# Performance work log

Hardware: AMD Instinct MI355X
Metric: run time of the kernel (lower is better)

Reference implementation:

```python
import jax, jax.numpy as jnp
import numpy as np
import math

B, H, S, D = 2, 16, 2048, 64

def setup_inputs() -> dict:
    key = jax.random.key(0)
    kq, kk, kv = jax.random.split(key, 3)
    Q = jax.random.normal(kq, (B, H, S, D), dtype=jnp.float32)
    K = jax.random.normal(kk, (B, H, S, D), dtype=jnp.float32)
    V = jax.random.normal(kv, (B, H, S, D), dtype=jnp.float32)
    causal_mask = jnp.tril(jnp.ones((S, S), dtype=bool))
    return {"Q": Q, "K": K, "V": V, "causal_mask": causal_mask}

def reference(Q, K, V, causal_mask):
    d_k = K.shape[-1]
    scores = jnp.einsum('bhqd,bhkd->bhqk', Q, K) / math.sqrt(d_k)
    scores = jnp.where(causal_mask, scores, -jnp.inf)
    probs = jax.nn.softmax(scores, axis=-1)
    return jnp.einsum('bhqk,bhkd->bhqd', probs, V)
```

## Files before the change

### kernel.cpp

```cpp
#include <hip/hip_runtime.h>
#include <math.h>


constexpr int kS   = 2048;
constexpr int kD   = 64;
constexpr int kBH  = 32;
constexpr int kPadP = 72;

typedef short short8 __attribute__((ext_vector_type(8)));
typedef float float4v __attribute__((ext_vector_type(4)));
typedef float float16v __attribute__((ext_vector_type(16)));
typedef unsigned int u32;
typedef unsigned short u16;

static __device__ inline u16 f2bf(float f) {
  union { float f; unsigned u; } v; v.f = f;
  unsigned r = v.u + 0x7FFF + ((v.u >> 16) & 1);
  return (u16)(r >> 16);
}

static __device__ inline short8 pack8(float4v a, float4v b) {
  short8 r;
  r[0] = (short)f2bf(a[0]); r[1] = (short)f2bf(a[1]);
  r[2] = (short)f2bf(a[2]); r[3] = (short)f2bf(a[3]);
  r[4] = (short)f2bf(b[0]); r[5] = (short)f2bf(b[1]);
  r[6] = (short)f2bf(b[2]); r[7] = (short)f2bf(b[3]);
  return r;
}

static __device__ inline void async_cp16(const void* g, void* l) {
  __builtin_amdgcn_global_load_lds(
      (const __attribute__((address_space(1))) u32*)g,
      (__attribute__((address_space(3))) u32*)l, 16, 0, 0);
}

static __device__ inline void swap32(u32 a, u32 b, u32& oa, u32& ob) {
#if __has_builtin(__builtin_amdgcn_permlane32_swap)
  auto r = __builtin_amdgcn_permlane32_swap(a, b, false, false);
  oa = r[0]; ob = r[1];
#else
  asm volatile("v_permlane32_swap_b32 %0, %1" : "+v"(a), "+v"(b));
  oa = a; ob = b;
#endif
}

__global__ __launch_bounds__(256)
void prep_kernel(const float* __restrict__ Q, const float* __restrict__ K,
                 const float* __restrict__ V,
                 u16* __restrict__ Qb, u16* __restrict__ Kb, u16* __restrict__ VT) {
  __shared__ u16 tile[64 * kPadP];
  const int tid = threadIdx.x;
  const int bh = blockIdx.y, st = blockIdx.x;
  const size_t ibase = (size_t)bh * kS * kD + (size_t)st * 64 * kD;
  const int r  = tid >> 2;
  const int c0 = (tid & 3) * 16;
  {
    const float scl = 0.125f * 1.44269504089f;
    const float* qp = Q + ibase + (size_t)r * kD + c0;
    float4v a = *(const float4v*)(qp);
    float4v b = *(const float4v*)(qp + 4);
    float4v c = *(const float4v*)(qp + 8);
    float4v d = *(const float4v*)(qp + 12);
    #pragma unroll
    for (int i = 0; i < 4; ++i) { a[i] *= scl; b[i] *= scl; c[i] *= scl; d[i] *= scl; }
    u16* dst = Qb + ibase + (size_t)r * kD + c0;
    *(short8*)dst       = pack8(a, b);
    *(short8*)(dst + 8) = pack8(c, d);
  }
  {
    const float* kp = K + ibase + (size_t)r * kD + c0;
    float4v a = *(const float4v*)(kp);
    float4v b = *(const float4v*)(kp + 4);
    float4v c = *(const float4v*)(kp + 8);
    float4v d = *(const float4v*)(kp + 12);
    u16* dst = Kb + ibase + (size_t)r * kD + c0;
    *(short8*)dst       = pack8(a, b);
    *(short8*)(dst + 8) = pack8(c, d);
  }
  {
    const float* vp = V + ibase + (size_t)r * kD + c0;
    float4v a = *(const float4v*)(vp);
    float4v b = *(const float4v*)(vp + 4);
    float4v c = *(const float4v*)(vp + 8);
    float4v d = *(const float4v*)(vp + 12);
    u16* t = &tile[r * kPadP + c0];
    *(short8*)t       = pack8(a, b);
    *(short8*)(t + 8) = pack8(c, d);
  }
  __syncthreads();
  {
    const int dd = tid >> 2;
    const int s0 = (tid & 3) * 16;
    short8 w0, w1;
    #pragma unroll
    for (int i = 0; i < 8; ++i) {
      w0[i] = (short)tile[(s0 + i) * kPadP + dd];
      w1[i] = (short)tile[(s0 + 8 + i) * kPadP + dd];
    }
    u16* vdst = VT + (size_t)bh * kD * kS + (size_t)dd * kS + st * 64 + s0;
    *(short8*)vdst       = w0;
    *(short8*)(vdst + 8) = w1;
  }
}

__global__ __launch_bounds__(256, 2)
void fattn_kernel(const u16* __restrict__ Qb, const u16* __restrict__ Kb,
                  const u16* __restrict__ VT,
                  u32* __restrict__ O0, u32* __restrict__ O1,
                  u32* __restrict__ O2, u32* __restrict__ O3,
                  float* __restrict__ Lp) {
  __shared__ __align__(16) u16 ldsK[2][4096];
  __shared__ __align__(16) u16 ldsV[2][4096];

  const int tid  = threadIdx.x;
  const int wave = tid >> 6;
  const int lane = tid & 63;
  const int l31  = lane & 31;
  const int h    = lane >> 5;

  const int bh = blockIdx.y;
  const int p  = blockIdx.x >> 2;
  const int z  = blockIdx.x & 3;
  const int qiA = p, qiB = 7 - p;
  const int nA  = 4 * p + 4;

  const size_t base  = (size_t)bh * kS * kD;
  const size_t vbase = (size_t)bh * kD * kS;

  const int lr  = lane >> 3;
  const int cxl = (lane & 7) ^ lr;
  const int offK0 = lr * 64   + cxl * 8;
  const int offV0 = lr * 2048 + cxl * 8;
  const unsigned hs16 = ((unsigned)(h ^ (l31 & 7))) * 16;

  u32* Od = (z == 0) ? O0 : (z == 1) ? O1 : (z == 2) ? O2 : O3;
  const int cB = 9 * z;
  const int cE = cB + 9;

  float16v zf;
  #pragma unroll
  for (int i = 0; i < 16; ++i) zf[i] = 0.f;

  int par = 0;
  for (int seg = 0; seg < 2; ++seg) {
    const int qi = seg ? qiB : qiA;
    int tb, te;
    if (seg == 0) { tb = min(cB, nA); te = min(cE, nA); }
    else          { tb = max(cB, nA) - nA; te = max(cE, nA) - nA; }
    const int wq0 = qi * 256 + wave * 64;

    short8 qf[2][4];
    #pragma unroll
    for (int g = 0; g < 2; ++g) {
      const u16* qp = Qb + base + (size_t)(wq0 + 32 * g + l31) * kD + h * 8;
      #pragma unroll
      for (int dk = 0; dk < 4; ++dk) qf[g][dk] = *(const short8*)(qp + dk * 16);
    }

    float16v acc[2][2];
    float lac[2] = {0.f, 0.f};
    #pragma unroll
    for (int g = 0; g < 2; ++g) { acc[g][0] = zf; acc[g][1] = zf; }

    if (tb < te) {
      {
        const u16* kg0 = Kb + base + (size_t)tb * 4096;
        const u16* vg0 = VT + vbase + tb * 64;
        const int b = par & 1;
        #pragma unroll
        for (int j = 0; j < 2; ++j) {
          const int g = wave + 4 * j;
          async_cp16(kg0 + g * 512 + offK0,           &ldsK[b][g * 512]);
          async_cp16(vg0 + (size_t)g * 16384 + offV0, &ldsV[b][g * 512]);
        }
      }
      for (int t = tb; t < te; ++t, ++par) {
        __syncthreads();
        if (t + 1 < te) {
          const u16* kg0 = Kb + base + (size_t)(t + 1) * 4096;
          const u16* vg0 = VT + vbase + (t + 1) * 64;
          const int b = (par + 1) & 1;
          #pragma unroll
          for (int j = 0; j < 2; ++j) {
            const int g = wave + 4 * j;
            async_cp16(kg0 + g * 512 + offK0,           &ldsK[b][g * 512]);
            async_cp16(vg0 + (size_t)g * 16384 + offV0, &ldsV[b][g * 512]);
          }
        }
        const char* KB = (const char*)ldsK[par & 1];
        const char* VB = (const char*)ldsV[par & 1];
        #pragma unroll
        for (int kt32 = 0; kt32 < 2; ++kt32) {
          const int ktb = t * 64 + kt32 * 32;
          if (ktb > wq0 + 63) break;

          const char* krow = KB + (kt32 * 32 + l31) * 128;
          short8 kf[4];
          #pragma unroll
          for (int dk = 0; dk < 4; ++dk)
            kf[dk] = *(const short8*)(krow + (((unsigned)(dk * 32)) ^ hs16));
          short8 vf[4];
          #pragma unroll
          for (int c = 0; c < 2; ++c) {
            const unsigned coff = ((unsigned)((kt32 * 4 + 2 * c) * 16)) ^ hs16;
            vf[2 * c]     = *(const short8*)(VB + l31 * 128 + coff);
            vf[2 * c + 1] = *(const short8*)(VB + (32 + l31) * 128 + coff);
          }

          #pragma unroll
          for (int g = 0; g < 2; ++g) {
            if (ktb > wq0 + 32 * g + 31) continue;

            __builtin_amdgcn_s_setprio(1);
            float16v s = __builtin_amdgcn_mfma_f32_32x32x16_bf16(kf[0], qf[g][0], zf, 0, 0, 0);
            s = __builtin_amdgcn_mfma_f32_32x32x16_bf16(kf[1], qf[g][1], s, 0, 0, 0);
            s = __builtin_amdgcn_mfma_f32_32x32x16_bf16(kf[2], qf[g][2], s, 0, 0, 0);
            s = __builtin_amdgcn_mfma_f32_32x32x16_bf16(kf[3], qf[g][3], s, 0, 0, 0);
            __builtin_amdgcn_s_setprio(0);

            if (ktb == wq0 + 32 * g) {
              const int qg = wq0 + 32 * g + l31;
              #pragma unroll
              for (int r = 0; r < 16; ++r) {
                const int kg = ktb + (r & 3) + 8 * (r >> 2) + 4 * h;
                if (kg > qg) s[r] = -1e30f;
              }
            }

            u32 pk[8];
            #pragma unroll
            for (int g2 = 0; g2 < 4; ++g2) {
              const u32 u0 = __float_as_uint(__builtin_amdgcn_exp2f(s[4 * g2 + 0]));
              const u32 u1 = __float_as_uint(__builtin_amdgcn_exp2f(s[4 * g2 + 1]));
              const u32 u2 = __float_as_uint(__builtin_amdgcn_exp2f(s[4 * g2 + 2]));
              const u32 u3 = __float_as_uint(__builtin_amdgcn_exp2f(s[4 * g2 + 3]));
              pk[2 * g2]     = __builtin_amdgcn_perm(u1, u0, 0x07060302u);
              pk[2 * g2 + 1] = __builtin_amdgcn_perm(u3, u2, 0x07060302u);
            }

            {
              float e[8];
              #pragma unroll
              for (int i = 0; i < 8; ++i)
                e[i] = __uint_as_float(pk[i] << 16)
                     + __uint_as_float(pk[i] & 0xFFFF0000u);
              e[0] += e[1]; e[2] += e[3]; e[4] += e[5]; e[6] += e[7];
              e[0] += e[2]; e[4] += e[6];
              lac[g] += e[0] + e[4];
            }

            #pragma unroll
            for (int c = 0; c < 2; ++c) {
              const int ga = 4 * c, gb = 4 * c + 2;
              union { u32 u[4]; short8 s8; } pf;
              swap32(pk[ga],     pk[gb],     pf.u[0], pf.u[2]);
              swap32(pk[ga + 1], pk[gb + 1], pf.u[1], pf.u[3]);
              __builtin_amdgcn_s_setprio(1);
              acc[g][0] = __builtin_amdgcn_mfma_f32_32x32x16_bf16(pf.s8, vf[2 * c],     acc[g][0], 0, 0, 0);
              acc[g][1] = __builtin_amdgcn_mfma_f32_32x32x16_bf16(pf.s8, vf[2 * c + 1], acc[g][1], 0, 0, 0);
              __builtin_amdgcn_s_setprio(0);
            }
          }
        }
      }
    }

    #pragma unroll
    for (int g = 0; g < 2; ++g) {
      #pragma unroll
      for (int r = 0; r < 16; ++r) {
        const int row = (r & 3) + 8 * (r >> 2) + 4 * h;
        const u32 w = (u32)f2bf(acc[g][0][r]) | ((u32)f2bf(acc[g][1][r]) << 16);
        Od[((size_t)bh * kS + wq0 + 32 * g + row) * 32 + l31] = w;
      }
      const float lt = lac[g] + __shfl_xor(lac[g], 32);
      if (lane < 32)
        Lp[(size_t)z * kBH * kS + (size_t)bh * kS + wq0 + 32 * g + lane] = lt;
    }
  }
}

__global__ __launch_bounds__(256)
void combine_kernel(const u32* __restrict__ O0, const u32* __restrict__ O1,
                    const u32* __restrict__ O2, const u32* __restrict__ O3,
                    const float* __restrict__ Lp, float* __restrict__ O) {
  const int idx = blockIdx.x * 256 + threadIdx.x;
  const int row = idx >> 5;
  const int j   = idx & 31;
  const int N = kBH * kS;
  const float l = Lp[row] + Lp[N + row] + Lp[2 * N + row] + Lp[3 * N + row];
  const float inv = 1.f / l;
  const u32 a = O0[idx], b = O1[idx], c = O2[idx], d = O3[idx];
  const float lo = __uint_as_float(a << 16) + __uint_as_float(b << 16)
                 + __uint_as_float(c << 16) + __uint_as_float(d << 16);
  const float hi = __uint_as_float(a & 0xFFFF0000u) + __uint_as_float(b & 0xFFFF0000u)
                 + __uint_as_float(c & 0xFFFF0000u) + __uint_as_float(d & 0xFFFF0000u);
  float* op = O + (size_t)row * kD;
  op[j]      = lo * inv;
  op[j + 32] = hi * inv;
}

extern "C" void kernel_launch(void* const* d_in, const int* in_sizes, int n_in,
                              void* d_out, int out_size, void* d_ws, size_t ws_size,
                              hipStream_t stream) {
  const float* Q = (const float*)d_in[0];
  const float* K = (const float*)d_in[1];
  const float* V = (const float*)d_in[2];
  float* O = (float*)d_out;

  const size_t nKV = (size_t)kBH * kS * kD;
  u16* Qb = (u16*)d_ws;
  u16* Kb = Qb + nKV;
  u16* VT = Kb + nKV;
  u32* O0 = (u32*)(VT + nKV);
  u32* O1 = O0 + nKV / 2;
  u32* O2 = O1 + nKV / 2;
  u32* O3 = O2 + nKV / 2;
  float* Lp = (float*)(O3 + nKV / 2);

  dim3 gprep(kS / 64, kBH);
  prep_kernel<<<gprep, 256, 0, stream>>>(Q, K, V, Qb, Kb, VT);
  dim3 grid(16, kBH);
  fattn_kernel<<<grid, 256, 0, stream>>>(Qb, Kb, VT, O0, O1, O2, O3, Lp);
  combine_kernel<<<(int)(kBH * kS * 32 / 256), 256, 0, stream>>>(O0, O1, O2, O3, Lp, O);
}
```

Baseline: 142.4 us.

## Replace split-KV partial outputs and combine kernel with per-block 64-row causal tiles

Work is now split so each block owns 64 query rows, ordered heaviest first. Within a block, the four waves divide into two query halves times two KV-parity halves, and the KV halves are reduced through LDS before the final normalized fp32 output is written directly. This removes the bf16 partial-output buffers, the partial row-sum buffers and the separate combine kernel launch, along with their global traffic and bf16 rounding of partials. In exchange each block streams K/V once for only 64 query rows, which doubles K/V loads relative to 256-row tiles. The grid grows to 1024 blocks of uneven length, and launch bounds rise to 3 blocks per SIMD.

```diff
diff --git a/kernel.cpp b/kernel.cpp
--- a/kernel.cpp
+++ b/kernel.cpp
@@ -103,12 +103,9 @@
   }
 }
 
-__global__ __launch_bounds__(256, 2)
+__global__ __launch_bounds__(256, 3)
 void fattn_kernel(const u16* __restrict__ Qb, const u16* __restrict__ Kb,
-                  const u16* __restrict__ VT,
-                  u32* __restrict__ O0, u32* __restrict__ O1,
-                  u32* __restrict__ O2, u32* __restrict__ O3,
-                  float* __restrict__ Lp) {
+                  const u16* __restrict__ VT, float* __restrict__ O) {
   __shared__ __align__(16) u16 ldsK[2][4096];
   __shared__ __align__(16) u16 ldsV[2][4096];
 
@@ -117,12 +114,12 @@
   const int lane = tid & 63;
   const int l31  = lane & 31;
   const int h    = lane >> 5;
+  const int g    = wave & 1;
+  const int kpar = wave >> 1;
 
   const int bh = blockIdx.y;
-  const int p  = blockIdx.x >> 2;
-  const int z  = blockIdx.x & 3;
-  const int qiA = p, qiB = 7 - p;
-  const int nA  = 4 * p + 4;
+  const int qb = 31 - blockIdx.x;
+  const int q0 = qb * 64;
 
   const size_t base  = (size_t)bh * kS * kD;
   const size_t vbase = (size_t)bh * kD * kS;
@@ -133,171 +130,146 @@
   const int offV0 = lr * 2048 + cxl * 8;
   const unsigned hs16 = ((unsigned)(h ^ (l31 & 7))) * 16;
 
-  u32* Od = (z == 0) ? O0 : (z == 1) ? O1 : (z == 2) ? O2 : O3;
-  const int cB = 9 * z;
-  const int cE = cB + 9;
-
   float16v zf;
   #pragma unroll
   for (int i = 0; i < 16; ++i) zf[i] = 0.f;
 
-  int par = 0;
-  for (int seg = 0; seg < 2; ++seg) {
-    const int qi = seg ? qiB : qiA;
-    int tb, te;
-    if (seg == 0) { tb = min(cB, nA); te = min(cE, nA); }
-    else          { tb = max(cB, nA) - nA; te = max(cE, nA) - nA; }
-    const int wq0 = qi * 256 + wave * 64;
-
-    short8 qf[2][4];
-    #pragma unroll
-    for (int g = 0; g < 2; ++g) {
-      const u16* qp = Qb + base + (size_t)(wq0 + 32 * g + l31) * kD + h * 8;
-      #pragma unroll
-      for (int dk = 0; dk < 4; ++dk) qf[g][dk] = *(const short8*)(qp + dk * 16);
-    }
-
-    float16v acc[2][2];
-    float lac[2] = {0.f, 0.f};
-    #pragma unroll
-    for (int g = 0; g < 2; ++g) { acc[g][0] = zf; acc[g][1] = zf; }
-
-    if (tb < te) {
+  short8 qf[4];
+  {
+    const u16* qp = Qb + base + (size_t)(q0 + 32 * g + l31) * kD + h * 8;
+    #pragma unroll
+    for (int dk = 0; dk < 4; ++dk) qf[dk] = *(const short8*)(qp + dk * 16);
+  }
+
+  float16v acc0 = zf, acc1 = zf;
+  float lac = 0.f;
+
+  const int kmax = 2 * qb + g;
+
+  {
+    const u16* kg0 = Kb + base;
+    const u16* vg0 = VT + vbase;
+    #pragma unroll
+    for (int j = 0; j < 2; ++j) {
+      const int gg = wave + 4 * j;
+      async_cp16(kg0 + gg * 512 + offK0,           &ldsK[0][gg * 512]);
+      async_cp16(vg0 + (size_t)gg * 16384 + offV0, &ldsV[0][gg * 512]);
+    }
+  }
+
+  for (int t = 0; t <= qb; ++t) {
+    __syncthreads();
+    if (t < qb) {
+      const u16* kg0 = Kb + base + (size_t)(t + 1) * 4096;
+      const u16* vg0 = VT + vbase + (t + 1) * 64;
+      const int b = (t + 1) & 1;
+      #pragma unroll
+      for (int j = 0; j < 2; ++j) {
+        const int gg = wave + 4 * j;
+        async_cp16(kg0 + gg * 512 + offK0,           &ldsK[b][gg * 512]);
+        async_cp16(vg0 + (size_t)gg * 16384 + offV0, &ldsV[b][gg * 512]);
+      }
+    }
+
+    const int K32 = 2 * t + kpar;
+    if (K32 <= kmax) {
+      const char* KB = (const char*)ldsK[t & 1];
+      const char* VB = (const char*)ldsV[t & 1];
+
+      const char* krow = KB + (kpar * 32 + l31) * 128;
+      short8 kf[4];
+      #pragma unroll
+      for (int dk = 0; dk < 4; ++dk)
+        kf[dk] = *(const short8*)(krow + (((unsigned)(dk * 32)) ^ hs16));
+      short8 vf[4];
+      #pragma unroll
+      for (int c = 0; c < 2; ++c) {
+        const unsigned coff = ((unsigned)((kpar * 4 + 2 * c) * 16)) ^ hs16;
+        vf[2 * c]     = *(const short8*)(VB + l31 * 128 + coff);
+        vf[2 * c + 1] = *(const short8*)(VB + (32 + l31) * 128 + coff);
+      }
+
+      __builtin_amdgcn_s_setprio(1);
+      float16v s = __builtin_amdgcn_mfma_f32_32x32x16_bf16(kf[0], qf[0], zf, 0, 0, 0);
+      s = __builtin_amdgcn_mfma_f32_32x32x16_bf16(kf[1], qf[1], s, 0, 0, 0);
+      s = __builtin_amdgcn_mfma_f32_32x32x16_bf16(kf[2], qf[2], s, 0, 0, 0);
+      s = __builtin_amdgcn_mfma_f32_32x32x16_bf16(kf[3], qf[3], s, 0, 0, 0);
+      __builtin_amdgcn_s_setprio(0);
+
+      if (K32 == kmax) {
+        const int ktb = t * 64 + kpar * 32;
+        const int qg  = q0 + 32 * g + l31;
+        #pragma unroll
+        for (int r = 0; r < 16; ++r) {
+          const int kg = ktb + (r & 3) + 8 * (r >> 2) + 4 * h;
+          if (kg > qg) s[r] = -1e30f;
+        }
+      }
+
+      u32 pk[8];
+      #pragma unroll
+      for (int g2 = 0; g2 < 4; ++g2) {
+        const u32 u0 = __float_as_uint(__builtin_amdgcn_exp2f(s[4 * g2 + 0]));
+        const u32 u1 = __float_as_uint(__builtin_amdgcn_exp2f(s[4 * g2 + 1]));
+        const u32 u2 = __float_as_uint(__builtin_amdgcn_exp2f(s[4 * g2 + 2]));
+        const u32 u3 = __float_as_uint(__builtin_amdgcn_exp2f(s[4 * g2 + 3]));
+        pk[2 * g2]     = __builtin_amdgcn_perm(u1, u0, 0x07060302u);
+        pk[2 * g2 + 1] = __builtin_amdgcn_perm(u3, u2, 0x07060302u);
+      }
+
       {
-        const u16* kg0 = Kb + base + (size_t)tb * 4096;
-        const u16* vg0 = VT + vbase + tb * 64;
-        const int b = par & 1;
+        float e[8];
         #pragma unroll
-        for (int j = 0; j < 2; ++j) {
-          const int g = wave + 4 * j;
-          async_cp16(kg0 + g * 512 + offK0,           &ldsK[b][g * 512]);
-          async_cp16(vg0 + (size_t)g * 16384 + offV0, &ldsV[b][g * 512]);
-        }
-      }
-      for (int t = tb; t < te; ++t, ++par) {
-        __syncthreads();
-        if (t + 1 < te) {
-          const u16* kg0 = Kb + base + (size_t)(t + 1) * 4096;
-          const u16* vg0 = VT + vbase + (t + 1) * 64;
-          const int b = (par + 1) & 1;
-          #pragma unroll
-          for (int j = 0; j < 2; ++j) {
-            const int g = wave + 4 * j;
-            async_cp16(kg0 + g * 512 + offK0,           &ldsK[b][g * 512]);
-            async_cp16(vg0 + (size_t)g * 16384 + offV0, &ldsV[b][g * 512]);
-          }
-        }
-        const char* KB = (const char*)ldsK[par & 1];
-        const char* VB = (const char*)ldsV[par & 1];
-        #pragma unroll
-        for (int kt32 = 0; kt32 < 2; ++kt32) {
-          const int ktb = t * 64 + kt32 * 32;
-          if (ktb > wq0 + 63) break;
-
-          const char* krow = KB + (kt32 * 32 + l31) * 128;
-          short8 kf[4];
-          #pragma unroll
-          for (int dk = 0; dk < 4; ++dk)
-            kf[dk] = *(const short8*)(krow + (((unsigned)(dk * 32)) ^ hs16));
-          short8 vf[4];
-          #pragma unroll
-          for (int c = 0; c < 2; ++c) {
-            const unsigned coff = ((unsigned)((kt32 * 4 + 2 * c) * 16)) ^ hs16;
-            vf[2 * c]     = *(const short8*)(VB + l31 * 128 + coff);
-            vf[2 * c + 1] = *(const short8*)(VB + (32 + l31) * 128 + coff);
-          }
-
-          #pragma unroll
-          for (int g = 0; g < 2; ++g) {
-            if (ktb > wq0 + 32 * g + 31) continue;
-
-            __builtin_amdgcn_s_setprio(1);
-            float16v s = __builtin_amdgcn_mfma_f32_32x32x16_bf16(kf[0], qf[g][0], zf, 0, 0, 0);
-            s = __builtin_amdgcn_mfma_f32_32x32x16_bf16(kf[1], qf[g][1], s, 0, 0, 0);
-            s = __builtin_amdgcn_mfma_f32_32x32x16_bf16(kf[2], qf[g][2], s, 0, 0, 0);
-            s = __builtin_amdgcn_mfma_f32_32x32x16_bf16(kf[3], qf[g][3], s, 0, 0, 0);
-            __builtin_amdgcn_s_setprio(0);
-
-            if (ktb == wq0 + 32 * g) {
-              const int qg = wq0 + 32 * g + l31;
-              #pragma unroll
-              for (int r = 0; r < 16; ++r) {
-                const int kg = ktb + (r & 3) + 8 * (r >> 2) + 4 * h;
-                if (kg > qg) s[r] = -1e30f;
-              }
-            }
-
-            u32 pk[8];
-            #pragma unroll
-            for (int g2 = 0; g2 < 4; ++g2) {
-              const u32 u0 = __float_as_uint(__builtin_amdgcn_exp2f(s[4 * g2 + 0]));
-              const u32 u1 = __float_as_uint(__builtin_amdgcn_exp2f(s[4 * g2 + 1]));
-              const u32 u2 = __float_as_uint(__builtin_amdgcn_exp2f(s[4 * g2 + 2]));
-              const u32 u3 = __float_as_uint(__builtin_amdgcn_exp2f(s[4 * g2 + 3]));
-              pk[2 * g2]     = __builtin_amdgcn_perm(u1, u0, 0x07060302u);
-              pk[2 * g2 + 1] = __builtin_amdgcn_perm(u3, u2, 0x07060302u);
-            }
-
-            {
-              float e[8];
-              #pragma unroll
-              for (int i = 0; i < 8; ++i)
-                e[i] = __uint_as_float(pk[i] << 16)
-                     + __uint_as_float(pk[i] & 0xFFFF0000u);
-              e[0] += e[1]; e[2] += e[3]; e[4] += e[5]; e[6] += e[7];
-              e[0] += e[2]; e[4] += e[6];
-              lac[g] += e[0] + e[4];
-            }
-
-            #pragma unroll
-            for (int c = 0; c < 2; ++c) {
-              const int ga = 4 * c, gb = 4 * c + 2;
-              union { u32 u[4]; short8 s8; } pf;
-              swap32(pk[ga],     pk[gb],     pf.u[0], pf.u[2]);
-              swap32(pk[ga + 1], pk[gb + 1], pf.u[1], pf.u[3]);
-              __builtin_amdgcn_s_setprio(1);
-              acc[g][0] = __builtin_amdgcn_mfma_f32_32x32x16_bf16(pf.s8, vf[2 * c],     acc[g][0], 0, 0, 0);
-              acc[g][1] = __builtin_amdgcn_mfma_f32_32x32x16_bf16(pf.s8, vf[2 * c + 1], acc[g][1], 0, 0, 0);
-              __builtin_amdgcn_s_setprio(0);
-            }
-          }
-        }
-      }
-    }
-
-    #pragma unroll
-    for (int g = 0; g < 2; ++g) {
-      #pragma unroll
-      for (int r = 0; r < 16; ++r) {
-        const int row = (r & 3) + 8 * (r >> 2) + 4 * h;
-        const u32 w = (u32)f2bf(acc[g][0][r]) | ((u32)f2bf(acc[g][1][r]) << 16);
-        Od[((size_t)bh * kS + wq0 + 32 * g + row) * 32 + l31] = w;
-      }
-      const float lt = lac[g] + __shfl_xor(lac[g], 32);
-      if (lane < 32)
-        Lp[(size_t)z * kBH * kS + (size_t)bh * kS + wq0 + 32 * g + lane] = lt;
-    }
-  }
-}
-
-__global__ __launch_bounds__(256)
-void combine_kernel(const u32* __restrict__ O0, const u32* __restrict__ O1,
-                    const u32* __restrict__ O2, const u32* __restrict__ O3,
-                    const float* __restrict__ Lp, float* __restrict__ O) {
-  const int idx = blockIdx.x * 256 + threadIdx.x;
-  const int row = idx >> 5;
-  const int j   = idx & 31;
-  const int N = kBH * kS;
-  const float l = Lp[row] + Lp[N + row] + Lp[2 * N + row] + Lp[3 * N + row];
-  const float inv = 1.f / l;
-  const u32 a = O0[idx], b = O1[idx], c = O2[idx], d = O3[idx];
-  const float lo = __uint_as_float(a << 16) + __uint_as_float(b << 16)
-                 + __uint_as_float(c << 16) + __uint_as_float(d << 16);
-  const float hi = __uint_as_float(a & 0xFFFF0000u) + __uint_as_float(b & 0xFFFF0000u)
-                 + __uint_as_float(c & 0xFFFF0000u) + __uint_as_float(d & 0xFFFF0000u);
-  float* op = O + (size_t)row * kD;
-  op[j]      = lo * inv;
-  op[j + 32] = hi * inv;
+        for (int i = 0; i < 8; ++i)
+          e[i] = __uint_as_float(pk[i] << 16)
+               + __uint_as_float(pk[i] & 0xFFFF0000u);
+        e[0] += e[1]; e[2] += e[3]; e[4] += e[5]; e[6] += e[7];
+        e[0] += e[2]; e[4] += e[6];
+        lac += e[0] + e[4];
+      }
+
+      #pragma unroll
+      for (int c = 0; c < 2; ++c) {
+        const int ga = 4 * c, gb = 4 * c + 2;
+        union { u32 u[4]; short8 s8; } pf;
+        swap32(pk[ga],     pk[gb],     pf.u[0], pf.u[2]);
+        swap32(pk[ga + 1], pk[gb + 1], pf.u[1], pf.u[3]);
+        __builtin_amdgcn_s_setprio(1);
+        acc0 = __builtin_amdgcn_mfma_f32_32x32x16_bf16(pf.s8, vf[2 * c],     acc0, 0, 0, 0);
+        acc1 = __builtin_amdgcn_mfma_f32_32x32x16_bf16(pf.s8, vf[2 * c + 1], acc1, 0, 0, 0);
+        __builtin_amdgcn_s_setprio(0);
+      }
+    }
+  }
+
+  __syncthreads();
+  float* SA = (float*)&ldsK[0][0];
+  float* SL = (float*)&ldsV[0][0];
+
+  const float lt = lac + __shfl_xor(lac, 32);
+  if (lane < 32) SL[kpar * 64 + g * 32 + lane] = lt;
+  if (kpar == 1) {
+    #pragma unroll
+    for (int r = 0; r < 16; ++r) {
+      const int row = (r & 3) + 8 * (r >> 2) + 4 * h;
+      SA[(g * 32 + row) * 64 + l31]      = acc0[r];
+      SA[(g * 32 + row) * 64 + 32 + l31] = acc1[r];
+    }
+  }
+  __syncthreads();
+  if (kpar == 0) {
+    #pragma unroll
+    for (int r = 0; r < 16; ++r) {
+      const int row = (r & 3) + 8 * (r >> 2) + 4 * h;
+      const float lsum = SL[g * 32 + row] + SL[64 + g * 32 + row];
+      const float inv  = 1.f / lsum;
+      const float o0 = (acc0[r] + SA[(g * 32 + row) * 64 + l31])      * inv;
+      const float o1 = (acc1[r] + SA[(g * 32 + row) * 64 + 32 + l31]) * inv;
+      float* op = O + ((size_t)bh * kS + q0 + 32 * g + row) * kD;
+      op[l31]      = o0;
+      op[l31 + 32] = o1;
+    }
+  }
 }
 
 extern "C" void kernel_launch(void* const* d_in, const int* in_sizes, int n_in,
@@ -312,15 +284,9 @@
   u16* Qb = (u16*)d_ws;
   u16* Kb = Qb + nKV;
   u16* VT = Kb + nKV;
-  u32* O0 = (u32*)(VT + nKV);
-  u32* O1 = O0 + nKV / 2;
-  u32* O2 = O1 + nKV / 2;
-  u32* O3 = O2 + nKV / 2;
-  float* Lp = (float*)(O3 + nKV / 2);
 
   dim3 gprep(kS / 64, kBH);
   prep_kernel<<<gprep, 256, 0, stream>>>(Q, K, V, Qb, Kb, VT);
-  dim3 grid(16, kBH);
-  fattn_kernel<<<grid, 256, 0, stream>>>(Qb, Kb, VT, O0, O1, O2, O3, Lp);
-  combine_kernel<<<(int)(kBH * kS * 32 / 256), 256, 0, stream>>>(O0, O1, O2, O3, Lp, O);
-}
+  dim3 grid(kS / 64, kBH);
+  fattn_kernel<<<grid, 256, 0, stream>>>(Qb, Kb, VT, O);
+}
```

Result: slower. 150.0 us (+5.3%).
